# Kernel tuning notes

Hardware: AMD Instinct MI355X
Metric: run time of the kernel (lower is better)

The kernel has to match this reference:

```python
import jax, jax.numpy as jnp
import numpy as np
from jax import lax

B, CIN, H, W = 8, 256, 64, 64
CC = 128          # corr_channels
COUT = 64         # out_channels
KH = KW = 5       # corr_kernel_size
SH = SW = 1       # corr_stride
PT, PB = KH // 2, (KH + 1) // 2 - 1   # pad='k'
PL, PR = KW // 2, (KW + 1) // 2 - 1


def setup_inputs() -> dict:
    key = jax.random.key(0)
    k1, k2, k3, k4, k5 = jax.random.split(key, 5)
    x = jax.random.normal(k1, (B, CIN, H, W), dtype=jnp.float32)
    w_ext = jax.random.normal(k2, (CC, CIN, 3, 3), dtype=jnp.float32) * 0.02
    b_ext = jax.random.normal(k3, (CC,), dtype=jnp.float32) * 0.02
    w_reg = jax.random.normal(k4, (COUT, CC, KH, KW), dtype=jnp.float32) * 0.02
    b_reg = jax.random.normal(k5, (COUT,), dtype=jnp.float32) * 0.02
    return {"x": x, "w_ext": w_ext, "b_ext": b_ext, "w_reg": w_reg, "b_reg": b_reg}


def _forward(x, w_ext, b_ext, w_reg, b_reg):
    # feature extraction: 3x3 conv, padding 1
    f = lax.conv_general_dilated(x, w_ext, (1, 1), ((1, 1), (1, 1)))
    f = f + b_ext[None, :, None, None]
    # local autocorrelation: multiply each window element by the window center, per channel
    fp = jnp.pad(f, ((0, 0), (0, 0), (PT, PB), (PL, PR)))
    nH = (fp.shape[2] - KH) // SH + 1
    nW = (fp.shape[3] - KW) // SW + 1
    center = fp[:, :, KH // 2:KH // 2 + nH * SH:SH, KW // 2:KW // 2 + nW * SW:SW]  # [B,CC,nH,nW]
    patches = jnp.stack(
        [fp[:, :, u:u + nH * SH:SH, v:v + nW * SW:SW] for u in range(KH) for v in range(KW)],
        axis=-1)  # [B,CC,nH,nW,KH*KW]
    corr = patches * center[..., None]  # [B,CC,nH,nW,KH*KW]
    out = jnp.einsum('bcijk,ock->bijo', corr, w_reg.reshape(COUT, CC, KH * KW))
    out = out + b_reg
    return out.transpose(0, 3, 1, 2)  # permute=True -> [B, COUT, nH, nW]


def reference(x, w_ext, b_ext, w_reg, b_reg):
    return _forward(x, w_ext, b_ext, w_reg, b_reg)
```

## Files before the change

kernel.cpp:

```cpp
#include <hip/hip_runtime.h>
#include <hip/hip_bf16.h>

#define B_    8
#define CIN_  256
#define CC_   128
#define COUT_ 64
#define HP_   68
#define HPX_  (HP_ * HP_)
#define XQW_  66
#define XQPX_ (XQW_ * XQW_)

typedef __attribute__((ext_vector_type(8))) short bh8;
typedef __attribute__((ext_vector_type(4))) float f4;

__device__ __forceinline__ ushort f2bf(float f) {
    uint u = __float_as_uint(f);
    return (ushort)((u + 0x7fffu + ((u >> 16) & 1u)) >> 16);
}
__device__ __forceinline__ float bf2f(ushort s) {
    return __uint_as_float(((uint)s) << 16);
}
__device__ __forceinline__ short f2bf_c(float f) {
    __hip_bfloat16 h = __float2bfloat16(f);
    short s;
    __builtin_memcpy(&s, &h, 2);
    return s;
}

#define NB_MISC 4264
__global__ __launch_bounds__(256) void prep_all(const float* __restrict__ x,
                                                const float* __restrict__ w_ext,
                                                const float* __restrict__ w_reg,
                                                short* __restrict__ wg,
                                                short* __restrict__ wa,
                                                ushort* __restrict__ fpad_t,
                                                ushort* __restrict__ xq,
                                                float* __restrict__ out) {
    __shared__ float xt[2][32][65];
    const int tid = threadIdx.x;
    if (blockIdx.x < NB_MISC) {
        int e = blockIdx.x * 256 + tid;
        if (e < 67584) {
            int seg = e & 15;
            int t = e >> 4;
            int b = t / 528, rp = t - b * 528;
            int i, j;
            if (rp < 136) { i = rp / 68; j = rp - (rp / 68) * 68; }
            else if (rp < 272) { int r = rp - 136; i = 66 + r / 68; j = r - (r / 68) * 68; }
            else { int r = rp - 272; i = 2 + (r >> 2); int c = r & 3; j = (c < 2) ? c : c + 64; }
            uint4 z; z.x = 0u; z.y = 0u; z.z = 0u; z.w = 0u;
            *(uint4*)&fpad_t[(((size_t)b * HPX_) + i * HP_ + j) * 128 + seg * 8] = z;
            return;
        }
        e -= 67584;
        if (e < 294912) {
            int ci = e & 31;
            int t  = e >> 5;
            int cc = t & 127;
            int t2 = t >> 7;
            int rs = t2 % 9, cb = t2 / 9;
            wg[e] = (short)f2bf(w_ext[(cc * CIN_ + cb * 32 + ci) * 9 + rs]);
            return;
        }
        e -= 294912;
        if (e < 204800) {
            int ci = e & 31;
            int o  = (e >> 5) & 63;
            int rest = e >> 11;
            int k = rest % 25, q = rest / 25;
            wa[e] = (short)f2bf(w_reg[(o * CC_ + q * 32 + ci) * 25 + k]);
            return;
        }
        e -= 204800;
        if (e < 524288) {
            float4 z; z.x = 0.f; z.y = 0.f; z.z = 0.f; z.w = 0.f;
            *(float4*)&out[(size_t)e * 4] = z;
        }
        return;
    }

    const int pid = blockIdx.x - NB_MISC;
    const int rp = pid % 33, cb = (pid / 33) & 7, b = pid / 264;

#pragma unroll
    for (int rr = 0; rr < 2; ++rr) {
        int y = rp * 2 + rr - 1;
        if ((unsigned)y < 64u) {
            int xx = tid & 63, wv = tid >> 6;
#pragma unroll
            for (int it = 0; it < 8; ++it) {
                int ci = it * 4 + wv;
                xt[rr][ci][xx] = x[(((size_t)(b * CIN_ + cb * 32 + ci)) * 64 + y) * 64 + xx];
            }
        }
    }
    __syncthreads();

    for (int e = tid; e < 528; e += 256) {
        int rr = e / 264, t = e - rr * 264;
        int hc = t >> 2, seg = t & 3;
        int y = rp * 2 + rr - 1, xx = hc - 1;
        uint pk[4] = {0u, 0u, 0u, 0u};
        if ((unsigned)y < 64u && (unsigned)xx < 64u) {
#pragma unroll
            for (int i = 0; i < 4; ++i) {
                uint lo = f2bf(xt[rr][seg * 8 + i * 2][xx]);
                uint hi = f2bf(xt[rr][seg * 8 + i * 2 + 1][xx]);
                pk[i] = lo | (hi << 16);
            }
        }
        uint4 v; v.x = pk[0]; v.y = pk[1]; v.z = pk[2]; v.w = pk[3];
        *(uint4*)&xq[((((size_t)(b * 8 + cb)) * XQPX_) + (rp * 2 + rr) * XQW_ + hc) * 32 + seg * 8] = v;
    }
}

__global__ __launch_bounds__(512)
__attribute__((amdgpu_waves_per_eu(2, 2)))
void conv3x3_mfma(const ushort* __restrict__ xq,
                  const short* __restrict__ wg,
                  const float* __restrict__ bext,
                  ushort* __restrict__ fpad_t) {
    __shared__ __align__(16) short xh[2][180 * 72];
    __shared__ __align__(16) short wlds[2][3 * 128 * 32];
    const int tid = threadIdx.x;
    const int lane = tid & 63, wv = tid >> 6;
    const int ch = wv >> 1, pg = wv & 1;
    const int j0 = blockIdx.x * 16, i0 = blockIdx.y * 8, b = blockIdx.z;
    const int l15 = lane & 15, kg = lane >> 4;
    const int cc0 = ch * 32;

    int abase[2];
#pragma unroll
    for (int mm = 0; mm < 2; ++mm) {
        int cc = cc0 + mm * 16 + l15;
        abase[mm] = cc * 32 + ((((cc >> 1) + kg) & 3) << 3);
    }
    int xb[4];
#pragma unroll
    for (int nn = 0; nn < 4; ++nn) {
        int px = pg * 64 + nn * 16 + l15, pi = px >> 4, pj = px & 15;
        xb[nn] = (pi * 18 + pj) * 72 + kg * 8;
    }
    int wdst[3]; int goff[3];
#pragma unroll
    for (int k = 0; k < 3; ++k) {
        int c = tid + k * 512;
        int cc = (c & 511) >> 2, kgc = c & 3;
        wdst[k] = (c >> 9) * 4096 + cc * 32 + ((((cc >> 1) + kgc) & 3) << 3);
        goff[k] = c * 8;
    }
    int xsrc[2], xdst[2];
#pragma unroll
    for (int k = 0; k < 2; ++k) {
        int c = tid + k * 512;
        int hp = c >> 2, seg = c & 3;
        int hr = hp / 18, hc = hp - hr * 18;
        xsrc[k] = ((i0 + hr) * XQW_ + (j0 + hc)) * 32 + seg * 8;
        xdst[k] = hp * 72 + seg * 8;
    }
    const bool x1ok = tid < 208;

    f4 acc[2][4] = {};

    {
#pragma unroll
        for (int k = 0; k < 3; ++k)
            *(bh8*)&wlds[0][wdst[k]] = *(const bh8*)(wg + goff[k]);
        const ushort* xbase = xq + (((size_t)(b * 8 + 0)) * XQPX_) * 32;
        *(bh8*)&xh[0][xdst[0]] = *(const bh8*)&xbase[xsrc[0]];
        if (x1ok) *(bh8*)&xh[0][xdst[1]] = *(const bh8*)&xbase[xsrc[1]];
    }
    __syncthreads();

    int p = 0;
#pragma unroll 1
    for (int cb = 0; cb < 8; ++cb) {
        const int xbuf = cb & 1;
#pragma unroll 1
        for (int g = 0; g < 3; ++g) {
            const int buf = p & 1;
            const bool wmore = (p < 23);
            const bool xmore = (g == 2) && (cb < 7);

            bh8 wreg[3];
            const short* gsrc = wg + (size_t)(wmore ? (p + 1) : 23) * 12288;
#pragma unroll
            for (int k = 0; k < 3; ++k)
                wreg[k] = *(const bh8*)(gsrc + goff[k]);
            bh8 xr0, xr1;
            if (xmore) {
                const ushort* xbase = xq + (((size_t)(b * 8 + cb + 1)) * XQPX_) * 32;
                xr0 = *(const bh8*)&xbase[xsrc[0]];
                if (x1ok) xr1 = *(const bh8*)&xbase[xsrc[1]];
            }

            const short* wb = wlds[buf];
#pragma unroll
            for (int s = 0; s < 3; ++s) {
                bh8 a[2], bb[4];
#pragma unroll
                for (int mm = 0; mm < 2; ++mm)
                    a[mm] = *(const bh8*)&wb[s * 4096 + abase[mm]];
#pragma unroll
                for (int nn = 0; nn < 4; ++nn)
                    bb[nn] = *(const bh8*)&xh[xbuf][xb[nn] + (g * 18 + s) * 72];
#pragma unroll
                for (int mm = 0; mm < 2; ++mm)
#pragma unroll
                    for (int nn = 0; nn < 4; ++nn)
                        acc[mm][nn] = __builtin_amdgcn_mfma_f32_16x16x32_bf16(
                            a[mm], bb[nn], acc[mm][nn], 0, 0, 0);
            }

            if (wmore) {
#pragma unroll
                for (int k = 0; k < 3; ++k)
                    *(bh8*)&wlds[buf ^ 1][wdst[k]] = wreg[k];
            }
            if (xmore) {
                *(bh8*)&xh[xbuf ^ 1][xdst[0]] = xr0;
                if (x1ok) *(bh8*)&xh[xbuf ^ 1][xdst[1]] = xr1;
            }
            __syncthreads();
            ++p;
        }
    }

#pragma unroll
    for (int mm = 0; mm < 2; ++mm) {
        const int ccb = cc0 + mm * 16 + kg * 4;
        float bv0 = bext[ccb + 0], bv1 = bext[ccb + 1];
        float bv2 = bext[ccb + 2], bv3 = bext[ccb + 3];
#pragma unroll
        for (int nn = 0; nn < 4; ++nn) {
            int px = pg * 64 + nn * 16 + l15, pi = px >> 4, pj = px & 15;
            size_t row = (size_t)b * HPX_ + (2 + i0 + pi) * HP_ + (2 + j0 + pj);
            uint lo = (uint)f2bf(acc[mm][nn][0] + bv0) | ((uint)f2bf(acc[mm][nn][1] + bv1) << 16);
            uint hi = (uint)f2bf(acc[mm][nn][2] + bv2) | ((uint)f2bf(acc[mm][nn][3] + bv3) << 16);
            uint2 pk; pk.x = lo; pk.y = hi;
            *(uint2*)&fpad_t[row * 128 + ccb] = pk;
        }
    }
}

__global__ __launch_bounds__(512)
__attribute__((amdgpu_waves_per_eu(2, 2)))
void autocorr_mfma(const ushort* __restrict__ ft,
                   const short* __restrict__ wA,
                   const float* __restrict__ breg,
                   float* __restrict__ out) {
    __shared__ __align__(16) short flds[400 * 72];
    __shared__ __align__(16) short wlds[2][5 * 64 * 32];
    const int tid = threadIdx.x;
    const int lane = tid & 63, wv = tid >> 6;
    const int j0 = blockIdx.x * 16, i0 = blockIdx.y * 16;
    const int b = blockIdx.z >> 1, h = blockIdx.z & 1;
    const int l15 = lane & 15, kg = lane >> 4;

    int abase[4];
#pragma unroll
    for (int mm = 0; mm < 4; ++mm) {
        int o = mm * 16 + l15;
        abase[mm] = o * 32 + ((((o >> 1) + kg) & 3) << 3);
    }
    int wdst[3]; int goff[3];
#pragma unroll
    for (int k = 0; k < 3; ++k) {
        int c = tid + k * 512;
        int o = (c & 255) >> 2, kgc = c & 3;
        wdst[k] = (c >> 8) * 2048 + o * 32 + ((((o >> 1) + kgc) & 3) << 3);
        goff[k] = c * 8;
    }
    const bool w3 = tid < 256;
    const short* wbase_g = wA + (size_t)h * 102400;

    for (int e = tid; e < 3200; e += 512) {
        int hp = e >> 3, seg = e & 7;
        int hr = hp / 20, hc = hp - hr * 20;
        const ushort* src = ft + ((size_t)b * HPX_ + (i0 + hr) * HP_ + (j0 + hc)) * 128 + (h * 8 + seg) * 8;
        *(bh8*)&flds[hp * 72 + seg * 8] = *(const bh8*)src;
    }
    *(bh8*)&wlds[0][wdst[0]] = *(const bh8*)(wbase_g + goff[0]);
    *(bh8*)&wlds[0][wdst[1]] = *(const bh8*)(wbase_g + goff[1]);
    if (w3) *(bh8*)&wlds[0][wdst[2]] = *(const bh8*)(wbase_g + goff[2]);
    __syncthreads();

    f4 acc[4][2] = {};
    int base_off[2], cen_off[2];
#pragma unroll
    for (int t = 0; t < 2; ++t) {
        int px = wv * 32 + t * 16 + l15;
        int pi = px >> 4, pj = px & 15;
        base_off[t] = (pi * 20 + pj) * 72 + kg * 8;
        cen_off[t]  = ((pi + 2) * 20 + (pj + 2)) * 72 + kg * 8;
    }

    int p = 0;
#pragma unroll 1
    for (int qq = 0; qq < 2; ++qq) {
        float cen[2][8];
#pragma unroll
        for (int t = 0; t < 2; ++t) {
            bh8 c8 = *(const bh8*)&flds[cen_off[t] + qq * 32];
#pragma unroll
            for (int jj = 0; jj < 8; ++jj) cen[t][jj] = bf2f((ushort)c8[jj]);
        }
#pragma unroll 1
        for (int u = 0; u < 5; ++u) {
            const int buf = p & 1;
            const bool wmore = (p < 9);

            bh8 wreg0, wreg1, wreg2;
            const short* gsrc = wbase_g + (size_t)(wmore ? (p + 1) : 9) * 10240;
            wreg0 = *(const bh8*)(gsrc + goff[0]);
            wreg1 = *(const bh8*)(gsrc + goff[1]);
            if (w3) wreg2 = *(const bh8*)(gsrc + goff[2]);

            const short* wb = wlds[buf];
#pragma unroll
            for (int v = 0; v < 5; ++v) {
                const int koff = (u * 20 + v) * 72;
                bh8 a[4];
#pragma unroll
                for (int mm = 0; mm < 4; ++mm)
                    a[mm] = *(const bh8*)&wb[v * 2048 + abase[mm]];
                bh8 bb[2];
#pragma unroll
                for (int t = 0; t < 2; ++t) {
                    bh8 s8 = *(const bh8*)&flds[base_off[t] + qq * 32 + koff];
#pragma unroll
                    for (int jj = 0; jj < 8; ++jj) {
                        float pr = bf2f((ushort)s8[jj]) * cen[t][jj];
                        bb[t][jj] = f2bf_c(pr);
                    }
                }
#pragma unroll
                for (int mm = 0; mm < 4; ++mm)
#pragma unroll
                    for (int t = 0; t < 2; ++t)
                        acc[mm][t] = __builtin_amdgcn_mfma_f32_16x16x32_bf16(
                            a[mm], bb[t], acc[mm][t], 0, 0, 0);
            }

            if (wmore) {
                *(bh8*)&wlds[buf ^ 1][wdst[0]] = wreg0;
                *(bh8*)&wlds[buf ^ 1][wdst[1]] = wreg1;
                if (w3) *(bh8*)&wlds[buf ^ 1][wdst[2]] = wreg2;
            }
            __syncthreads();
            ++p;
        }
    }

#pragma unroll
    for (int mm = 0; mm < 4; ++mm) {
#pragma unroll
        for (int reg = 0; reg < 4; ++reg) {
            int o = mm * 16 + kg * 4 + reg;
            float bv = (h == 0) ? breg[o] : 0.f;
#pragma unroll
            for (int t = 0; t < 2; ++t) {
                int px = wv * 32 + t * 16 + l15, pi = px >> 4, pj = px & 15;
                float* dst = &out[(((size_t)(b * COUT_ + o)) * 64 + i0 + pi) * 64 + j0 + pj];
                __hip_atomic_fetch_add(dst, acc[mm][t][reg] + bv,
                                       __ATOMIC_RELAXED, __HIP_MEMORY_SCOPE_AGENT);
            }
        }
    }
}

extern "C" void kernel_launch(void* const* d_in, const int* in_sizes, int n_in,
                              void* d_out, int out_size, void* d_ws, size_t ws_size,
                              hipStream_t stream) {
    const float* x     = (const float*)d_in[0];
    const float* w_ext = (const float*)d_in[1];
    const float* b_ext = (const float*)d_in[2];
    const float* w_reg = (const float*)d_in[3];
    const float* b_reg = (const float*)d_in[4];
    float* out = (float*)d_out;

    char* ws = (char*)d_ws;
    const size_t FPADT_BYTES = (size_t)B_ * HPX_ * 128 * 2;
    const size_t WG_BYTES    = (size_t)8 * 9 * 128 * 32 * 2;
    const size_t WA_BYTES    = (size_t)4 * 25 * 64 * 32 * 2;
    ushort* fpad_t = (ushort*)ws;
    short*  wgq    = (short*)(ws + FPADT_BYTES);
    short*  wa     = (short*)(ws + FPADT_BYTES + WG_BYTES);
    ushort* xq     = (ushort*)(ws + FPADT_BYTES + WG_BYTES + WA_BYTES);

    prep_all<<<NB_MISC + 33 * 8 * 8, 256, 0, stream>>>(x, w_ext, w_reg, wgq, wa, fpad_t, xq, out);

    dim3 cgrid(4, 8, 8);
    conv3x3_mfma<<<cgrid, 512, 0, stream>>>(xq, wgq, b_ext, fpad_t);
    dim3 agrid(4, 4, 16);
    autocorr_mfma<<<agrid, 512, 0, stream>>>(fpad_t, wa, b_reg, out);
}
```

Baseline: 74.41 us.

## Stage full per-channel-group weight slab in LDS, cut per-step barriers

The autocorrelation kernel no longer double-buffers weights one row (u) at a time with a barrier after every row. It now loads all 25 kernel taps' weights for one 32-channel group into a larger LDS buffer. The second group's weights are prefetched into registers and written between the two qq passes, so barriers drop from ten to about two. The inner u loop is fully unrolled and the initial feature and weight loads are batched into registers before the LDS stores. The cost is a much larger LDS footprint (about 100KB for weights plus the feature tile) and many more live registers, which could lower occupancy or cause spills under waves_per_eu(2,2).

New measurement: 82.84 us. 11.3% more time.

```diff
diff --git a/kernel.cpp b/kernel.cpp
--- a/kernel.cpp
+++ b/kernel.cpp
@@ -250,7 +250,7 @@
                    const float* __restrict__ breg,
                    float* __restrict__ out) {
     __shared__ __align__(16) short flds[400 * 72];
-    __shared__ __align__(16) short wlds[2][5 * 64 * 32];
+    __shared__ __align__(16) short wlds[25 * 2048];
     const int tid = threadIdx.x;
     const int lane = tid & 63, wv = tid >> 6;
     const int j0 = blockIdx.x * 16, i0 = blockIdx.y * 16;
@@ -263,27 +263,48 @@
         int o = mm * 16 + l15;
         abase[mm] = o * 32 + ((((o >> 1) + kg) & 3) << 3);
     }
-    int wdst[3]; int goff[3];
-#pragma unroll
-    for (int k = 0; k < 3; ++k) {
-        int c = tid + k * 512;
-        int o = (c & 255) >> 2, kgc = c & 3;
-        wdst[k] = (c >> 8) * 2048 + o * 32 + ((((o >> 1) + kgc) & 3) << 3);
-        goff[k] = c * 8;
-    }
-    const bool w3 = tid < 256;
     const short* wbase_g = wA + (size_t)h * 102400;
 
-    for (int e = tid; e < 3200; e += 512) {
-        int hp = e >> 3, seg = e & 7;
-        int hr = hp / 20, hc = hp - hr * 20;
-        const ushort* src = ft + ((size_t)b * HPX_ + (i0 + hr) * HP_ + (j0 + hc)) * 128 + (h * 8 + seg) * 8;
-        *(bh8*)&flds[hp * 72 + seg * 8] = *(const bh8*)src;
-    }
-    *(bh8*)&wlds[0][wdst[0]] = *(const bh8*)(wbase_g + goff[0]);
-    *(bh8*)&wlds[0][wdst[1]] = *(const bh8*)(wbase_g + goff[1]);
-    if (w3) *(bh8*)&wlds[0][wdst[2]] = *(const bh8*)(wbase_g + goff[2]);
+    bh8 fr[7]; bh8 wr[13];
+#pragma unroll
+    for (int k = 0; k < 7; ++k) {
+        int e = tid + k * 512;
+        if (k < 6 || tid < 128) {
+            int hp = e >> 3, seg = e & 7;
+            int hr = hp / 20, hc = hp - hr * 20;
+            fr[k] = *(const bh8*)(ft + ((size_t)b * HPX_ + (i0 + hr) * HP_ + (j0 + hc)) * 128 + (h * 8 + seg) * 8);
+        }
+    }
+#pragma unroll
+    for (int k = 0; k < 13; ++k) {
+        int e = tid + k * 512;
+        if (k < 12 || tid < 256)
+            wr[k] = *(const bh8*)(wbase_g + e * 8);
+    }
+#pragma unroll
+    for (int k = 0; k < 7; ++k) {
+        int e = tid + k * 512;
+        if (k < 6 || tid < 128) {
+            int hp = e >> 3, seg = e & 7;
+            *(bh8*)&flds[hp * 72 + seg * 8] = fr[k];
+        }
+    }
+#pragma unroll
+    for (int k = 0; k < 13; ++k) {
+        int e = tid + k * 512;
+        if (k < 12 || tid < 256) {
+            int kk = e >> 8, o = (e & 255) >> 2, kgc = e & 3;
+            *(bh8*)&wlds[kk * 2048 + o * 32 + ((((o >> 1) + kgc) & 3) << 3)] = wr[k];
+        }
+    }
     __syncthreads();
+
+#pragma unroll
+    for (int k = 0; k < 13; ++k) {
+        int e = tid + k * 512;
+        if (k < 12 || tid < 256)
+            wr[k] = *(const bh8*)(wbase_g + 51200 + e * 8);
+    }
 
     f4 acc[4][2] = {};
     int base_off[2], cen_off[2];
@@ -295,7 +316,6 @@
         cen_off[t]  = ((pi + 2) * 20 + (pj + 2)) * 72 + kg * 8;
     }
 
-    int p = 0;
 #pragma unroll 1
     for (int qq = 0; qq < 2; ++qq) {
         float cen[2][8];
@@ -305,25 +325,16 @@
 #pragma unroll
             for (int jj = 0; jj < 8; ++jj) cen[t][jj] = bf2f((ushort)c8[jj]);
         }
-#pragma unroll 1
+#pragma unroll
         for (int u = 0; u < 5; ++u) {
-            const int buf = p & 1;
-            const bool wmore = (p < 9);
-
-            bh8 wreg0, wreg1, wreg2;
-            const short* gsrc = wbase_g + (size_t)(wmore ? (p + 1) : 9) * 10240;
-            wreg0 = *(const bh8*)(gsrc + goff[0]);
-            wreg1 = *(const bh8*)(gsrc + goff[1]);
-            if (w3) wreg2 = *(const bh8*)(gsrc + goff[2]);
-
-            const short* wb = wlds[buf];
 #pragma unroll
             for (int v = 0; v < 5; ++v) {
                 const int koff = (u * 20 + v) * 72;
+                const int kidx = u * 5 + v;
                 bh8 a[4];
 #pragma unroll
                 for (int mm = 0; mm < 4; ++mm)
-                    a[mm] = *(const bh8*)&wb[v * 2048 + abase[mm]];
+                    a[mm] = *(const bh8*)&wlds[kidx * 2048 + abase[mm]];
                 bh8 bb[2];
 #pragma unroll
                 for (int t = 0; t < 2; ++t) {
@@ -341,14 +352,19 @@
                         acc[mm][t] = __builtin_amdgcn_mfma_f32_16x16x32_bf16(
                             a[mm], bb[t], acc[mm][t], 0, 0, 0);
             }
-
-            if (wmore) {
-                *(bh8*)&wlds[buf ^ 1][wdst[0]] = wreg0;
-                *(bh8*)&wlds[buf ^ 1][wdst[1]] = wreg1;
-                if (w3) *(bh8*)&wlds[buf ^ 1][wdst[2]] = wreg2;
-            }
+        }
+
+        if (qq == 0) {
             __syncthreads();
-            ++p;
+#pragma unroll
+            for (int k = 0; k < 13; ++k) {
+                int e = tid + k * 512;
+                if (k < 12 || tid < 256) {
+                    int kk = e >> 8, o = (e & 255) >> 2, kgc = e & 3;
+                    *(bh8*)&wlds[kk * 2048 + o * 32 + ((((o >> 1) + kgc) & 3) << 3)] = wr[k];
+                }
+            }
+            __syncthreads();
         }
     }
 
```
